# Optimization experiments

Hardware: AMD Instinct MI355X
Metric: run time of the kernel (lower is better)

## Reference

```python
import jax, jax.numpy as jnp
import numpy as np

DROPOUT_P = 0.3


def setup_inputs() -> dict:
    key = jax.random.key(0)
    kq, kk, kv, ks = jax.random.split(key, 4)
    B, Sq, Skv, D = 32, 2048, 2048, 128
    q = jax.random.normal(kq, (B, Sq, D), dtype=jnp.float32)
    k = jax.random.normal(kk, (B, Skv, D), dtype=jnp.float32)
    v = jax.random.normal(kv, (B, Skv, D), dtype=jnp.float32)
    # torch.randint(low=1, high=256, size=[B,1]) -> per-batch positive scale
    scale_factor = jax.random.randint(ks, (B, 1, 1), 1, 256).astype(jnp.float32)
    return {"q": q, "k": k, "v": v, "scale_factor": scale_factor}


def reference(q, k, v, scale_factor):
    # qk = q @ k^T ; div by scale_factor**-1 == multiply by scale_factor
    scores = jnp.einsum("bqd,bkd->bqk", q, k) * scale_factor  # [B,Sq,Skv]
    attn = jax.nn.softmax(scores, axis=-1)
    # dropout with fixed key (deterministic reference for torch F.dropout)
    keep_p = 1.0 - DROPOUT_P
    dk = jax.random.key(42)
    keep = jax.random.bernoulli(dk, keep_p, attn.shape)
    attn_d = jnp.where(keep, attn / keep_p, 0.0)
    return jnp.einsum("bqk,bkd->bqd", attn_d, v)
```

## Files before the change

kernel.cpp:

```cpp
#include <hip/hip_runtime.h>
#include <stdint.h>


namespace {

constexpr int Bb  = 32;
constexpr int SQ  = 2048;
constexpr int SKV = 2048;
constexpr int DH  = 128;
constexpr int KT  = 32;
constexpr int NKT = SKV / KT;
constexpr int TILE_F16 = 12288;
constexpr size_t WS_NEED = (size_t)Bb * NKT * TILE_F16 * 2;
constexpr int PSTR = KT + 8;

typedef _Float16 f16x8 __attribute__((ext_vector_type(8)));
typedef _Float16 f16x4 __attribute__((ext_vector_type(4)));
typedef float    f32x4 __attribute__((ext_vector_type(4)));

__device__ __forceinline__ uint32_t rotl32(uint32_t x, int d) {
  return (x << d) | (x >> (32 - d));
}

__device__ __forceinline__ uint32_t jax_random_bits(uint32_t i) {
  constexpr uint32_t K0 = 0u;
  constexpr uint32_t K1 = 42u;
  constexpr uint32_t K2 = 0x1BD11BDAu ^ K0 ^ K1;
  uint32_t x0 = K0;
  uint32_t x1 = i + K1;
#define TF4(a,b,c,d) \
  x0 += x1; x1 = rotl32(x1,a); x1 ^= x0; \
  x0 += x1; x1 = rotl32(x1,b); x1 ^= x0; \
  x0 += x1; x1 = rotl32(x1,c); x1 ^= x0; \
  x0 += x1; x1 = rotl32(x1,d); x1 ^= x0;
  TF4(13,15,26,6)   x0 += K1; x1 += K2 + 1u;
  TF4(17,29,16,24)  x0 += K2; x1 += K0 + 2u;
  TF4(13,15,26,6)   x0 += K0; x1 += K1 + 3u;
  TF4(17,29,16,24)  x0 += K1; x1 += K2 + 4u;
  TF4(13,15,26,6)   x0 += K2; x1 += K0 + 5u;
#undef TF4
  return x0 ^ x1;
}

__device__ __forceinline__ bool jax_keep(uint32_t i) {
  const uint32_t fb = (jax_random_bits(i) >> 9) | 0x3f800000u;
  return (__uint_as_float(fb) - 1.0f) < 0.7f;
}

__device__ __forceinline__ _Float16 hi16(float x) { return (_Float16)x; }
__device__ __forceinline__ _Float16 lo16(float x) {
  return (_Float16)(x - (float)((_Float16)x));
}

}

__global__ __launch_bounds__(256) void prep_tile(const float* __restrict__ Kg,
                                                 const float* __restrict__ Vg,
                                                 _Float16* __restrict__ ws) {
  __shared__ alignas(16) float sT[KT][DH + 4];

  const int tid  = threadIdx.x;
  const int b    = blockIdx.x >> 6;
  const int kt   = blockIdx.x & 63;
  _Float16* tile = ws + (size_t)(b * NKT + kt) * TILE_F16;

  {
    const float* kb = Kg + ((size_t)b * SKV + kt * KT) * DH;
#pragma unroll
    for (int rep = 0; rep < 4; ++rep) {
      const int idx = tid + 256 * rep;
      const int row = idx >> 5;
      const int c4  = idx & 31;
      *reinterpret_cast<float4*>(&sT[row][4 * c4]) =
          *reinterpret_cast<const float4*>(kb + (size_t)row * DH + 4 * c4);
    }
  }
  __syncthreads();
#pragma unroll
  for (int rep = 0; rep < 2; ++rep) {
    const int task = tid + 256 * rep;
    const int lane = task & 63;
    const int f    = task >> 6;
    const int ks   = f >> 1;
    const int ct   = f & 1;
    const int cl   = lane & 15;
    const int g8   = (lane >> 4) * 8;
    const float* src = &sT[ct * 16 + cl][ks * 32 + g8];
    f16x8 h, l;
#pragma unroll
    for (int j = 0; j < 8; ++j) { h[j] = hi16(src[j]); l[j] = lo16(src[j]); }
    *reinterpret_cast<f16x8*>(tile + f * 512 + lane * 8)        = h;
    *reinterpret_cast<f16x8*>(tile + 4096 + f * 512 + lane * 8) = l;
  }
  __syncthreads();

  {
    const float* vb = Vg + ((size_t)b * SKV + kt * KT) * DH;
#pragma unroll
    for (int rep = 0; rep < 4; ++rep) {
      const int idx = tid + 256 * rep;
      const int row = idx >> 5;
      const int c4  = idx & 31;
      *reinterpret_cast<float4*>(&sT[row][4 * c4]) =
          *reinterpret_cast<const float4*>(vb + (size_t)row * DH + 4 * c4);
    }
  }
  __syncthreads();
#pragma unroll
  for (int rep = 0; rep < 2; ++rep) {
    const int task = tid + 256 * rep;
    const int lane = task & 63;
    const int dt   = task >> 6;
    const int cl   = lane & 15;
    const int g8   = (lane >> 4) * 8;
    f16x8 w;
#pragma unroll
    for (int j = 0; j < 8; ++j)
      w[j] = (_Float16)sT[g8 + j][dt * 16 + cl];
    *reinterpret_cast<f16x8*>(tile + 8192 + dt * 512 + lane * 8) = w;
  }
}

__global__ __launch_bounds__(256, 3) void fused_attn5(
    const float* __restrict__ Qg, const _Float16* __restrict__ Wk,
    const float* __restrict__ Sg, float* __restrict__ Og)
{
  __shared__ alignas(16) _Float16 sStage[TILE_F16];
  __shared__ alignas(16) _Float16 sP[4][16][PSTR];

  const int tid  = threadIdx.x;
  const int wid  = tid >> 6;
  const int lane = tid & 63;
  const int cl   = lane & 15;
  const int g8   = (lane >> 4) * 8;
  const int r0   = (lane >> 4) * 4;

  const int b  = blockIdx.x >> 5;
  const int q0 = (blockIdx.x & 31) * 64;
  const float scale = Sg[b];

  f16x8 qhi[4], qlo[4];
  {
    const float* qp = Qg + ((size_t)b * SQ + q0 + wid * 16 + cl) * DH + g8;
#pragma unroll
    for (int ks = 0; ks < 4; ++ks) {
      const float4 a0 = *reinterpret_cast<const float4*>(qp + 32 * ks);
      const float4 a1 = *reinterpret_cast<const float4*>(qp + 32 * ks + 4);
      const float xs[8] = {a0.x, a0.y, a0.z, a0.w, a1.x, a1.y, a1.z, a1.w};
#pragma unroll
      for (int j = 0; j < 8; ++j) { qhi[ks][j] = hi16(xs[j]); qlo[ks][j] = lo16(xs[j]); }
    }
  }

  float m_run[4], l_run[4], alpha[4];
  f32x4 oacc[8];
#pragma unroll
  for (int i = 0; i < 4; ++i) { m_run[i] = -INFINITY; l_run[i] = 0.0f; }
#pragma unroll
  for (int dt = 0; dt < 8; ++dt) oacc[dt] = (f32x4){0.f, 0.f, 0.f, 0.f};

  for (int kt = 0; kt < NKT; ++kt) {
    __syncthreads();

    const uint32_t* tsrc =
        reinterpret_cast<const uint32_t*>(Wk + (size_t)(b * NKT + kt) * TILE_F16);
#pragma unroll
    for (int c = 0; c < 6; ++c) {
      const int j = wid + 4 * c;
      __builtin_amdgcn_global_load_lds(tsrc + j * 256 + lane * 4,
          reinterpret_cast<uint32_t*>(&sStage[j * 512]), 16, 0, 0);
    }
    __syncthreads();

    f32x4 sacc[2];
#pragma unroll
    for (int ct = 0; ct < 2; ++ct) {
      sacc[ct] = (f32x4){0.f, 0.f, 0.f, 0.f};
#pragma unroll
      for (int ks = 0; ks < 4; ++ks) {
        const int f = ks * 2 + ct;
        const f16x8 bhi = *reinterpret_cast<const f16x8*>(&sStage[f * 512 + lane * 8]);
        const f16x8 blo = *reinterpret_cast<const f16x8*>(&sStage[4096 + f * 512 + lane * 8]);
        sacc[ct] = __builtin_amdgcn_mfma_f32_16x16x32_f16(qhi[ks], bhi, sacc[ct], 0, 0, 0);
        sacc[ct] = __builtin_amdgcn_mfma_f32_16x16x32_f16(qlo[ks], bhi, sacc[ct], 0, 0, 0);
        sacc[ct] = __builtin_amdgcn_mfma_f32_16x16x32_f16(qhi[ks], blo, sacc[ct], 0, 0, 0);
      }
    }

    bool anyalpha = false;
#pragma unroll
    for (int i = 0; i < 4; ++i) {
      float mraw = fmaxf(sacc[0][i], sacc[1][i]);
#pragma unroll
      for (int off = 8; off >= 1; off >>= 1)
        mraw = fmaxf(mraw, __shfl_xor(mraw, off, 64));
      const float mt = mraw * scale;

      if (mt >= m_run[i] - 9.21f) {
        const float mnew = fmaxf(m_run[i], mt);
        alpha[i] = __expf(m_run[i] - mnew);
        m_run[i] = mnew;
        const int qrow = q0 + wid * 16 + r0 + i;
        const uint32_t rowbase =
            ((uint32_t)b * (uint32_t)SQ + (uint32_t)qrow) * (uint32_t)SKV
            + (uint32_t)(kt * KT);
        float ps = 0.0f;
#pragma unroll
        for (int ct = 0; ct < 2; ++ct) {
          const float p = __expf(sacc[ct][i] * scale - mnew);
          ps += p;
          const bool keep = jax_keep(rowbase + (uint32_t)(16 * ct + cl));
          sP[wid][r0 + i][16 * ct + cl] = keep ? (_Float16)(p * (1.0f / 0.7f))
                                               : (_Float16)0.0f;
        }
#pragma unroll
        for (int off = 8; off >= 1; off >>= 1)
          ps += __shfl_xor(ps, off, 64);
        l_run[i] = l_run[i] * alpha[i] + ps;
        anyalpha |= (alpha[i] != 1.0f);
      } else {
        alpha[i] = 1.0f;
#pragma unroll
        for (int ct = 0; ct < 2; ++ct)
          sP[wid][r0 + i][16 * ct + cl] = (_Float16)0.0f;
      }
    }

    if (anyalpha) {
#pragma unroll
      for (int dt = 0; dt < 8; ++dt)
#pragma unroll
        for (int i = 0; i < 4; ++i) oacc[dt][i] *= alpha[i];
    }

    const f16x8 pa = *reinterpret_cast<const f16x8*>(&sP[wid][cl][g8]);
#pragma unroll
    for (int dt = 0; dt < 8; ++dt) {
      const f16x8 bv = *reinterpret_cast<const f16x8*>(
          &sStage[8192 + dt * 512 + lane * 8]);
      oacc[dt] = __builtin_amdgcn_mfma_f32_16x16x32_f16(pa, bv, oacc[dt], 0, 0, 0);
    }
  }

#pragma unroll
  for (int i = 0; i < 4; ++i) {
    const float inv_l = 1.0f / l_run[i];
    float* op = Og + ((size_t)b * SQ + (size_t)(q0 + wid * 16 + r0 + i)) * DH + cl;
#pragma unroll
    for (int dt = 0; dt < 8; ++dt)
      op[16 * dt] = oacc[dt][i] * inv_l;
  }
}

namespace {
constexpr int FKT  = 64;
constexpr int KSTR = DH + 8;
constexpr int VSTR = FKT + 8;
constexpr int FPSTR = FKT + 8;
}

__global__ __launch_bounds__(256, 2) void fused_attn_fb(
    const float* __restrict__ Qg, const float* __restrict__ Kg,
    const float* __restrict__ Vg, const float* __restrict__ Sg,
    float* __restrict__ Og)
{
  __shared__ alignas(16) _Float16 sKhi[FKT][KSTR];
  __shared__ alignas(16) _Float16 sKlo[FKT][KSTR];
  __shared__ alignas(16) _Float16 sVt[DH][VSTR];
  __shared__ alignas(16) _Float16 sP[4][16][FPSTR];

  const int tid  = threadIdx.x;
  const int wid  = tid >> 6;
  const int lane = tid & 63;
  const int cl   = lane & 15;
  const int g8   = (lane >> 4) * 8;
  const int r0   = (lane >> 4) * 4;

  const int b  = blockIdx.x >> 5;
  const int q0 = (blockIdx.x & 31) * 64;
  const float scale = Sg[b];

  f16x8 qhi[4], qlo[4];
  {
    const float* qp = Qg + ((size_t)b * SQ + q0 + wid * 16 + cl) * DH + g8;
#pragma unroll
    for (int ks = 0; ks < 4; ++ks) {
      const float4 a0 = *reinterpret_cast<const float4*>(qp + 32 * ks);
      const float4 a1 = *reinterpret_cast<const float4*>(qp + 32 * ks + 4);
      const float xs[8] = {a0.x, a0.y, a0.z, a0.w, a1.x, a1.y, a1.z, a1.w};
#pragma unroll
      for (int j = 0; j < 8; ++j) { qhi[ks][j] = hi16(xs[j]); qlo[ks][j] = lo16(xs[j]); }
    }
  }

  float m_run[4], l_run[4], alpha[4];
  f32x4 oacc[8];
#pragma unroll
  for (int i = 0; i < 4; ++i) { m_run[i] = -INFINITY; l_run[i] = 0.0f; }
#pragma unroll
  for (int dt = 0; dt < 8; ++dt) oacc[dt] = (f32x4){0.f, 0.f, 0.f, 0.f};

  for (int k0 = 0; k0 < SKV; k0 += FKT) {
    __syncthreads();
#pragma unroll
    for (int rep = 0; rep < 8; ++rep) {
      const int idx = tid + 256 * rep;
      const int row = idx >> 5;
      const int c4  = idx & 31;
      const float4 t = *reinterpret_cast<const float4*>(
          Kg + ((size_t)b * SKV + k0 + row) * DH + 4 * c4);
      f16x4 h4, l4;
      h4[0] = hi16(t.x); l4[0] = lo16(t.x);
      h4[1] = hi16(t.y); l4[1] = lo16(t.y);
      h4[2] = hi16(t.z); l4[2] = lo16(t.z);
      h4[3] = hi16(t.w); l4[3] = lo16(t.w);
      *reinterpret_cast<f16x4*>(&sKhi[row][4 * c4]) = h4;
      *reinterpret_cast<f16x4*>(&sKlo[row][4 * c4]) = l4;
    }
#pragma unroll
    for (int rep = 0; rep < 2; ++rep) {
      const int u  = tid + 256 * rep;
      const int du = u & 31;
      const int ku = u >> 5;
      const float* vb = Vg + ((size_t)b * SKV + k0 + 4 * ku) * DH + 4 * du;
      float4 t[4];
#pragma unroll
      for (int j = 0; j < 4; ++j)
        t[j] = *reinterpret_cast<const float4*>(vb + (size_t)j * DH);
#pragma unroll
      for (int dd = 0; dd < 4; ++dd) {
        const float v0 = (&t[0].x)[dd], v1 = (&t[1].x)[dd],
                    v2 = (&t[2].x)[dd], v3 = (&t[3].x)[dd];
        f16x4 w4 = {(_Float16)v0, (_Float16)v1, (_Float16)v2, (_Float16)v3};
        *reinterpret_cast<f16x4*>(&sVt[4 * du + dd][4 * ku]) = w4;
      }
    }
    __syncthreads();

    f32x4 sacc[4];
#pragma unroll
    for (int ct = 0; ct < 4; ++ct) {
      sacc[ct] = (f32x4){0.f, 0.f, 0.f, 0.f};
#pragma unroll
      for (int ks = 0; ks < 4; ++ks) {
        const f16x8 bhi = *reinterpret_cast<const f16x8*>(&sKhi[16 * ct + cl][32 * ks + g8]);
        const f16x8 blo = *reinterpret_cast<const f16x8*>(&sKlo[16 * ct + cl][32 * ks + g8]);
        sacc[ct] = __builtin_amdgcn_mfma_f32_16x16x32_f16(qhi[ks], bhi, sacc[ct], 0, 0, 0);
        sacc[ct] = __builtin_amdgcn_mfma_f32_16x16x32_f16(qlo[ks], bhi, sacc[ct], 0, 0, 0);
        sacc[ct] = __builtin_amdgcn_mfma_f32_16x16x32_f16(qhi[ks], blo, sacc[ct], 0, 0, 0);
      }
    }

    bool anyalpha = false;
#pragma unroll
    for (int i = 0; i < 4; ++i) {
      float mraw = fmaxf(fmaxf(sacc[0][i], sacc[1][i]), fmaxf(sacc[2][i], sacc[3][i]));
#pragma unroll
      for (int off = 8; off >= 1; off >>= 1)
        mraw = fmaxf(mraw, __shfl_xor(mraw, off, 64));
      const float mt = mraw * scale;
      if (mt >= m_run[i] - 9.21f) {
        const float mnew = fmaxf(m_run[i], mt);
        alpha[i] = __expf(m_run[i] - mnew);
        m_run[i] = mnew;
        const int qrow = q0 + wid * 16 + r0 + i;
        const uint32_t rowbase =
            ((uint32_t)b * (uint32_t)SQ + (uint32_t)qrow) * (uint32_t)SKV + (uint32_t)k0;
        float ps = 0.0f;
#pragma unroll
        for (int ct = 0; ct < 4; ++ct) {
          const float p = __expf(sacc[ct][i] * scale - mnew);
          ps += p;
          const bool keep = jax_keep(rowbase + (uint32_t)(16 * ct + cl));
          sP[wid][r0 + i][16 * ct + cl] = keep ? (_Float16)(p * (1.0f / 0.7f))
                                               : (_Float16)0.0f;
        }
#pragma unroll
        for (int off = 8; off >= 1; off >>= 1)
          ps += __shfl_xor(ps, off, 64);
        l_run[i] = l_run[i] * alpha[i] + ps;
        anyalpha |= (alpha[i] != 1.0f);
      } else {
        alpha[i] = 1.0f;
#pragma unroll
        for (int ct = 0; ct < 4; ++ct)
          sP[wid][r0 + i][16 * ct + cl] = (_Float16)0.0f;
      }
    }

    if (anyalpha) {
#pragma unroll
      for (int dt = 0; dt < 8; ++dt)
#pragma unroll
        for (int i = 0; i < 4; ++i) oacc[dt][i] *= alpha[i];
    }
#pragma unroll
    for (int ks2 = 0; ks2 < 2; ++ks2) {
      const f16x8 pa = *reinterpret_cast<const f16x8*>(&sP[wid][cl][32 * ks2 + g8]);
#pragma unroll
      for (int dt = 0; dt < 8; ++dt) {
        const f16x8 bv = *reinterpret_cast<const f16x8*>(&sVt[16 * dt + cl][32 * ks2 + g8]);
        oacc[dt] = __builtin_amdgcn_mfma_f32_16x16x32_f16(pa, bv, oacc[dt], 0, 0, 0);
      }
    }
  }

#pragma unroll
  for (int i = 0; i < 4; ++i) {
    const float inv_l = 1.0f / l_run[i];
    float* op = Og + ((size_t)b * SQ + (size_t)(q0 + wid * 16 + r0 + i)) * DH + cl;
#pragma unroll
    for (int dt = 0; dt < 8; ++dt)
      op[16 * dt] = oacc[dt][i] * inv_l;
  }
}

extern "C" void kernel_launch(void* const* d_in, const int* in_sizes, int n_in,
                              void* d_out, int out_size, void* d_ws, size_t ws_size,
                              hipStream_t stream) {
  (void)in_sizes; (void)n_in; (void)out_size;
  const float* q  = (const float*)d_in[0];
  const float* k  = (const float*)d_in[1];
  const float* v  = (const float*)d_in[2];
  const float* sc = (const float*)d_in[3];
  float* out = (float*)d_out;

  if (ws_size >= WS_NEED) {
    _Float16* ws = (_Float16*)d_ws;
    prep_tile<<<dim3(Bb * NKT), dim3(256), 0, stream>>>(k, v, ws);
    fused_attn5<<<dim3(Bb * (SQ / 64)), dim3(256), 0, stream>>>(q, ws, sc, out);
  } else {
    fused_attn_fb<<<dim3(Bb * (SQ / 64)), dim3(256), 0, stream>>>(q, k, v, sc, out);
  }
}
```

Measured before the change: 392.0 us.

## Double-buffer K/V LDS staging tiles to overlap global loads with MFMA

Makes the LDS staging buffer two tiles deep and prefetches the next K/V tile with global_load_lds while the current tile is consumed. Explicit s_waitcnt vmcnt and raw barriers replace the two __syncthreads per iteration. The aim is to hide global-to-LDS latency behind the QK and PV MFMA work. LDS use grows by about 24 KB per block, which may lower occupancy below the 3 blocks per CU set by launch bounds.

New measurement: 500.1 us. 1.28x slower.

```diff
diff --git a/kernel.cpp b/kernel.cpp
--- a/kernel.cpp
+++ b/kernel.cpp
@@ -125,7 +125,7 @@
     const float* __restrict__ Qg, const _Float16* __restrict__ Wk,
     const float* __restrict__ Sg, float* __restrict__ Og)
 {
-  __shared__ alignas(16) _Float16 sStage[TILE_F16];
+  __shared__ alignas(16) _Float16 sStage[2][TILE_F16];
   __shared__ alignas(16) _Float16 sP[4][16][PSTR];
 
   const int tid  = threadIdx.x;
@@ -159,18 +159,41 @@
 #pragma unroll
   for (int dt = 0; dt < 8; ++dt) oacc[dt] = (f32x4){0.f, 0.f, 0.f, 0.f};
 
-  for (int kt = 0; kt < NKT; ++kt) {
-    __syncthreads();
-
-    const uint32_t* tsrc =
-        reinterpret_cast<const uint32_t*>(Wk + (size_t)(b * NKT + kt) * TILE_F16);
+  const uint32_t* wbase =
+      reinterpret_cast<const uint32_t*>(Wk + (size_t)b * NKT * TILE_F16);
+
+  {
+    const uint32_t* tsrc = wbase;
 #pragma unroll
     for (int c = 0; c < 6; ++c) {
       const int j = wid + 4 * c;
       __builtin_amdgcn_global_load_lds(tsrc + j * 256 + lane * 4,
-          reinterpret_cast<uint32_t*>(&sStage[j * 512]), 16, 0, 0);
-    }
-    __syncthreads();
+          reinterpret_cast<uint32_t*>(&sStage[0][j * 512]), 16, 0, 0);
+    }
+  }
+
+  for (int kt = 0; kt < NKT; ++kt) {
+    const int cur = kt & 1;
+
+    __builtin_amdgcn_s_barrier();
+    asm volatile("" ::: "memory");
+
+    if (kt + 1 < NKT) {
+      const uint32_t* tsrc = wbase + (size_t)(kt + 1) * (TILE_F16 / 2);
+#pragma unroll
+      for (int c = 0; c < 6; ++c) {
+        const int j = wid + 4 * c;
+        __builtin_amdgcn_global_load_lds(tsrc + j * 256 + lane * 4,
+            reinterpret_cast<uint32_t*>(&sStage[cur ^ 1][j * 512]), 16, 0, 0);
+      }
+      asm volatile("s_waitcnt vmcnt(6)" ::: "memory");
+    } else {
+      asm volatile("s_waitcnt vmcnt(0)" ::: "memory");
+    }
+    __builtin_amdgcn_s_barrier();
+    asm volatile("" ::: "memory");
+
+    const _Float16* st = sStage[cur];
 
     f32x4 sacc[2];
 #pragma unroll
@@ -179,8 +202,8 @@
 #pragma unroll
       for (int ks = 0; ks < 4; ++ks) {
         const int f = ks * 2 + ct;
-        const f16x8 bhi = *reinterpret_cast<const f16x8*>(&sStage[f * 512 + lane * 8]);
-        const f16x8 blo = *reinterpret_cast<const f16x8*>(&sStage[4096 + f * 512 + lane * 8]);
+        const f16x8 bhi = *reinterpret_cast<const f16x8*>(&st[f * 512 + lane * 8]);
+        const f16x8 blo = *reinterpret_cast<const f16x8*>(&st[4096 + f * 512 + lane * 8]);
         sacc[ct] = __builtin_amdgcn_mfma_f32_16x16x32_f16(qhi[ks], bhi, sacc[ct], 0, 0, 0);
         sacc[ct] = __builtin_amdgcn_mfma_f32_16x16x32_f16(qlo[ks], bhi, sacc[ct], 0, 0, 0);
         sacc[ct] = __builtin_amdgcn_mfma_f32_16x16x32_f16(qhi[ks], blo, sacc[ct], 0, 0, 0);
@@ -237,7 +260,7 @@
 #pragma unroll
     for (int dt = 0; dt < 8; ++dt) {
       const f16x8 bv = *reinterpret_cast<const f16x8*>(
-          &sStage[8192 + dt * 512 + lane * 8]);
+          &st[8192 + dt * 512 + lane * 8]);
       oacc[dt] = __builtin_amdgcn_mfma_f32_16x16x32_f16(pa, bv, oacc[dt], 0, 0, 0);
     }
   }
```
